# Optimization experiments

Measured on AMD Instinct MI355X. Metric: run time of the kernel, lower is better.

Reference implementation:

```python
import jax, jax.numpy as jnp
import numpy as np

EMB = 2048
N_HEADS = 16
HEAD_DIM = EMB // N_HEADS
ROPE_BASE = 10000.0


def _rope_cos_sin(seq_len, head_dim, dtype):
    inv_freq = 1.0 / (ROPE_BASE ** (jnp.arange(0, head_dim, 2, dtype=jnp.float32) / head_dim))
    t = jnp.arange(seq_len, dtype=jnp.float32)
    freqs = jnp.einsum('s,d->sd', t, inv_freq)          # [S, head_dim/2]
    emb = jnp.concatenate([freqs, freqs], axis=-1)       # [S, head_dim]
    return jnp.cos(emb).astype(dtype), jnp.sin(emb).astype(dtype)


def _rotate_half(x):
    x1, x2 = jnp.split(x, 2, axis=-1)
    return jnp.concatenate([-x2, x1], axis=-1)


def _apply_rope(x, cos, sin):
    # x: [B, H, S, D]; cos/sin: [S, D]
    return x * cos[None, None, :, :] + _rotate_half(x) * sin[None, None, :, :]


def setup_inputs() -> dict:
    key = jax.random.key(0)
    k1, k2, k3 = jax.random.split(key, 3)
    B, S = 4, 2048
    x = jax.random.normal(k1, (B, S, EMB), dtype=jnp.float32)
    # Additive causal mask: 0 on/below diagonal, -1e9 above.
    causal = jnp.triu(jnp.full((S, S), -1e9, dtype=jnp.float32), k=1)
    att_mask = causal[None, None, :, :]
    Wqkv = jax.random.normal(k2, (3 * EMB, EMB), dtype=jnp.float32) * (EMB ** -0.5)
    Wout = jax.random.normal(k3, (EMB, EMB), dtype=jnp.float32) * (EMB ** -0.5)
    return {"x": x, "att_mask": att_mask, "Wqkv": Wqkv, "Wout": Wout}


def reference(x, att_mask, Wqkv, Wout):
    B, S, E = x.shape
    qkv = jnp.einsum('bse,fe->bsf', x, Wqkv)             # [B, S, 3E]
    q, k, v = jnp.split(qkv, 3, axis=-1)
    def to_heads(t):
        return t.reshape(B, S, N_HEADS, HEAD_DIM).transpose(0, 2, 1, 3)  # [B,H,S,D]
    q, k, v = to_heads(q), to_heads(k), to_heads(v)
    cos, sin = _rope_cos_sin(S, HEAD_DIM, x.dtype)
    q = _apply_rope(q, cos, sin)
    k = _apply_rope(k, cos, sin)
    scaling = HEAD_DIM ** -0.5
    dots = jnp.einsum('bhqd,bhkd->bhqk', q, k) * scaling
    dots = dots + att_mask
    attn = jax.nn.softmax(dots, axis=-1)
    out = jnp.einsum('bhqk,bhkd->bhqd', attn, v)         # [B,H,S,D]
    out = out.transpose(0, 2, 1, 3).reshape(B, S, E)
    return jnp.einsum('bse,fe->bsf', out, Wout)
```

## Files before the change

kernel.cpp:

```cpp
#include <hip/hip_runtime.h>
#include <stdint.h>

typedef __attribute__((ext_vector_type(8))) short short8_t;
typedef __attribute__((ext_vector_type(4))) float f32x4;

__device__ __forceinline__ short f2bf(float f) {
  union { float f; uint32_t u; } v; v.f = f;
  uint32_t r = v.u + 0x7FFFu + ((v.u >> 16) & 1u);
  return (short)(r >> 16);
}
__device__ __forceinline__ float bf2f(short s) {
  union { uint32_t u; float f; } v; v.u = ((uint32_t)(uint16_t)s) << 16; return v.f;
}
__device__ __forceinline__ void gld16(const void* g, void* l) {
  __builtin_amdgcn_global_load_lds((const __attribute__((address_space(1))) void*)g,
                                   (__attribute__((address_space(3))) void*)l, 16, 0, 0);
}

__global__ __launch_bounds__(256) void conv_kernel(const float* __restrict__ in,
                                                   short* __restrict__ out, int n4) {
  int i = blockIdx.x * 256 + threadIdx.x;
  const int stride = gridDim.x * 256;
  for (; i < n4; i += stride) {
    float4 v = reinterpret_cast<const float4*>(in)[i];
    short4 o;
    o.x = f2bf(v.x); o.y = f2bf(v.y); o.z = f2bf(v.z); o.w = f2bf(v.w);
    reinterpret_cast<short4*>(out)[i] = o;
  }
}

__device__ __forceinline__ void storeC(float* C, size_t i, float v) { C[i] = v; }
__device__ __forceinline__ void storeC(short* C, size_t i, float v) { C[i] = f2bf(v); }

template <typename OT>
__global__ __launch_bounds__(256) void gemm_bt(const short* __restrict__ A,
                                               const short* __restrict__ B,
                                               OT* __restrict__ C, int M, int N, int K,
                                               int nbx) {
  __shared__ __align__(16) short Al[128 * 32];
  __shared__ __align__(16) short Bl[128 * 32];
  const int tid = threadIdx.x, lane = tid & 63, w = tid >> 6;
  const int wr = w >> 1, wc = w & 1;
  const int c = lane & 15, g4 = lane >> 4;
  const int lin = (blockIdx.x & 7) * ((int)gridDim.x >> 3) + ((int)blockIdx.x >> 3);
  const int bx = lin % nbx, by = lin / nbx;
  const size_t m0 = (size_t)by * 128, n0 = (size_t)bx * 128;
  const size_t Kb = (size_t)K * 2;
  const char* Ab = (const char*)A + m0 * Kb;
  const char* Bb = (const char*)B + n0 * Kb;
  f32x4 acc[4][4] = {};
  const int nk = K >> 5;
  for (int ks = 0; ks < nk; ++ks) {
    const int kb = ks * 64;
#pragma unroll
    for (int i = 0; i < 2; ++i) {
      const int L = ((w * 2 + i) << 10) + lane * 16;
      const int row = L >> 6, inner = L & 63;
      gld16(Ab + (size_t)row * Kb + kb + inner, (char*)Al + ((w * 2 + i) << 10));
      gld16(Bb + (size_t)row * Kb + kb + inner, (char*)Bl + ((w * 2 + i) << 10));
    }
    __syncthreads();
    short8_t af[4], bfr[4];
#pragma unroll
    for (int m = 0; m < 4; ++m)
      af[m] = *(const short8_t*)&Al[(wr * 64 + m * 16 + c) * 32 + g4 * 8];
#pragma unroll
    for (int n = 0; n < 4; ++n)
      bfr[n] = *(const short8_t*)&Bl[(wc * 64 + n * 16 + c) * 32 + g4 * 8];
    __builtin_amdgcn_s_setprio(1);
#pragma unroll
    for (int m = 0; m < 4; ++m)
#pragma unroll
      for (int n = 0; n < 4; ++n)
        acc[m][n] = __builtin_amdgcn_mfma_f32_16x16x32_bf16(af[m], bfr[n], acc[m][n], 0, 0, 0);
    __builtin_amdgcn_s_setprio(0);
    __syncthreads();
  }
#pragma unroll
  for (int m = 0; m < 4; ++m)
#pragma unroll
    for (int n = 0; n < 4; ++n) {
      const size_t col = n0 + wc * 64 + n * 16 + c;
      const size_t rb = m0 + wr * 64 + m * 16 + g4 * 4;
#pragma unroll
      for (int r = 0; r < 4; ++r) storeC(C, (rb + r) * (size_t)N + col, acc[m][n][r]);
    }
}

__global__ __launch_bounds__(256) void rope_kernel(short* __restrict__ qkv) {
  const int g = blockIdx.x * 256 + threadIdx.x;
  const int jg = g & 7;
  const int h = (g >> 3) & 15;
  const int bs = g >> 7;
  const int s = bs & 2047;
  const size_t base = (size_t)bs * 6144 + 2048 + h * 128 + jg * 8;
  short8_t lo = *(short8_t*)&qkv[base];
  short8_t hi = *(short8_t*)&qkv[base + 64];
  short8_t olo, ohi;
#pragma unroll
  for (int t = 0; t < 8; ++t) {
    const int j = jg * 8 + t;
    const float inv = exp2f((float)j * -0.20762050593046f);
    float sn, cn;
    sincosf((float)s * inv, &sn, &cn);
    const float a = bf2f(lo[t]), b = bf2f(hi[t]);
    olo[t] = f2bf(a * cn - b * sn);
    ohi[t] = f2bf(b * cn + a * sn);
  }
  *(short8_t*)&qkv[base] = olo;
  *(short8_t*)&qkv[base + 64] = ohi;
}

__global__ __launch_bounds__(256) void vt_kernel(const short* __restrict__ qkv,
                                                 short* __restrict__ vt) {
  __shared__ __align__(16) short Vl[64][128];
  const int g = blockIdx.x;
  const int st = g & 31, bh = g >> 5;
  const int h = bh & 15, b = bh >> 4;
  const int t = threadIdx.x;
  const int s0 = st * 64;
#pragma unroll
  for (int p = 0; p < 4; ++p) {
    const int idx = p * 256 + t;
    const int row = idx >> 4, c16 = idx & 15;
    short8_t v = *(const short8_t*)&qkv[(size_t)(b * 2048 + s0 + row) * 6144 + 4096 + h * 128 + c16 * 8];
    *(short8_t*)&Vl[row][c16 * 8] = v;
  }
  __syncthreads();
  const size_t obase = ((size_t)(b * 16 + h) * 128) * 2048;
#pragma unroll
  for (int i = 0; i < 8; ++i) {
    const int idx = t * 8 + i;
    const int d = idx >> 4, sq = idx & 15;
    short4 o;
    o.x = Vl[sq * 4 + 0][d];
    o.y = Vl[sq * 4 + 1][d];
    o.z = Vl[sq * 4 + 2][d];
    o.w = Vl[sq * 4 + 3][d];
    *(short4*)&vt[obase + (size_t)d * 2048 + s0 + sq * 4] = o;
  }
}

__global__ __launch_bounds__(256) void attn_kernel(const short* __restrict__ qkv,
                                                   const short* __restrict__ vt,
                                                   short* __restrict__ o) {
  __shared__ __align__(16) short Kl[2][64 * 128];
  __shared__ __align__(16) short Vl[2][128 * 64];
  __shared__ __align__(16) short Pl[4][16 * 72];
  const int tid = threadIdx.x, lane = tid & 63, w = tid >> 6;
  const int c = lane & 15, g4 = lane >> 4;
  const int blk = blockIdx.x;
  const int xcd = blk & 7;
  const int l = blk >> 3;
  const int bh = xcd * 8 + (l >> 5);
  const int h = bh & 15, b = bh >> 4;
  const int q0 = (31 - (l & 31)) * 64;
  const int srow = q0 + w * 16 + c;

  short8_t qf[4];
  {
    const size_t qr = ((size_t)b * 2048 + srow) * 6144 + h * 128;
    float fl[4][8];
#pragma unroll
    for (int dc = 0; dc < 4; ++dc) {
      short8_t rawv = *(const short8_t*)&qkv[qr + dc * 32 + g4 * 8];
#pragma unroll
      for (int t = 0; t < 8; ++t) fl[dc][t] = bf2f(rawv[t]);
    }
#pragma unroll
    for (int pd = 0; pd < 2; ++pd)
#pragma unroll
      for (int t = 0; t < 8; ++t) {
        const int j = pd * 32 + g4 * 8 + t;
        const float inv = exp2f((float)j * -0.20762050593046f);
        float sn, cn;
        sincosf((float)srow * inv, &sn, &cn);
        const float a = fl[pd][t], bb = fl[pd + 2][t];
        fl[pd][t] = a * cn - bb * sn;
        fl[pd + 2][t] = bb * cn + a * sn;
      }
#pragma unroll
    for (int dc = 0; dc < 4; ++dc) {
      short8_t q8;
#pragma unroll
      for (int t = 0; t < 8; ++t) q8[t] = f2bf(fl[dc][t]);
      qf[dc] = q8;
    }
  }

  f32x4 acc_o[8] = {};
  float rs[4] = {0.f, 0.f, 0.f, 0.f};
  const float scale2 = 0.12751875222364685f;
  const char* Kbase = (const char*)qkv + ((size_t)b * 2048 * 6144 + 2048 + h * 128) * 2;
  const char* Vbase = (const char*)vt + ((size_t)(b * 16 + h) * 128 * 2048) * 2;

  const char* kq[4];
  const char* vq[4];
#pragma unroll
  for (int i = 0; i < 4; ++i) {
    const int L = ((w * 4 + i) << 10) + lane * 16;
    {
      const int row = L >> 8, inner = L & 255;
      kq[i] = Kbase + (size_t)row * 12288 + (inner ^ ((row & 7) << 4));
    }
    {
      const int row = L >> 7, inner = L & 127;
      vq[i] = Vbase + (size_t)row * 4096 + (inner ^ ((row & 7) << 4));
    }
  }
  auto stage = [&](int buf, int kv0) {
#pragma unroll
    for (int i = 0; i < 4; ++i) {
      gld16(kq[i] + (size_t)kv0 * 12288, (char*)Kl + (buf << 14) + ((w * 4 + i) << 10));
      gld16(vq[i] + (size_t)kv0 * 2, (char*)Vl + (buf << 14) + ((w * 4 + i) << 10));
    }
  };

  stage(0, 0);
  __syncthreads();
  int cur = 0;
  for (int kv0 = 0; kv0 <= q0; kv0 += 64) {
    if (kv0 + 64 <= q0) stage(cur ^ 1, kv0 + 64);
    const char* Kb = (const char*)Kl + (cur << 14);
    const char* Vb = (const char*)Vl + (cur << 14);
    const bool diag = (kv0 == q0);
    float p[4][4];
#pragma unroll
    for (int kt = 0; kt < 4; ++kt) {
      f32x4 s4 = {};
      const int krow = kt * 16 + c;
      __builtin_amdgcn_s_setprio(1);
#pragma unroll
      for (int dc = 0; dc < 4; ++dc) {
        const int inner = (dc * 64 + g4 * 16) ^ ((krow & 7) << 4);
        short8_t kf = *(const short8_t*)(Kb + krow * 256 + inner);
        s4 = __builtin_amdgcn_mfma_f32_16x16x32_bf16(qf[dc], kf, s4, 0, 0, 0);
      }
      __builtin_amdgcn_s_setprio(0);
#pragma unroll
      for (int r = 0; r < 4; ++r) {
        float v = s4[r] * scale2 - 8.0f;
        if (diag) {
          const int kc = kv0 + kt * 16 + c;
          const int qr2 = q0 + w * 16 + g4 * 4 + r;
          if (kc > qr2) v = -1e30f;
        }
        const float pe = exp2f(v);
        p[kt][r] = pe;
        rs[r] += pe;
      }
    }
#pragma unroll
    for (int kt = 0; kt < 4; ++kt)
#pragma unroll
      for (int r = 0; r < 4; r += 2) {
        uint32_t pk;
        asm("v_cvt_pk_bf16_f32 %0, %1, %2" : "=v"(pk) : "v"(p[kt][r]), "v"(p[kt][r + 1]));
        Pl[w][(g4 * 4 + r) * 72 + kt * 16 + c] = (short)(pk & 0xffffu);
        Pl[w][(g4 * 4 + r + 1) * 72 + kt * 16 + c] = (short)(pk >> 16);
      }
#pragma unroll
    for (int kk = 0; kk < 2; ++kk) {
      short8_t pf = *(const short8_t*)&Pl[w][c * 72 + kk * 32 + g4 * 8];
      __builtin_amdgcn_s_setprio(1);
#pragma unroll
      for (int dt = 0; dt < 8; ++dt) {
        const int vrow = dt * 16 + c;
        const int inner = (kk * 64 + g4 * 16) ^ ((vrow & 7) << 4);
        short8_t vf = *(const short8_t*)(Vb + vrow * 128 + inner);
        acc_o[dt] = __builtin_amdgcn_mfma_f32_16x16x32_bf16(pf, vf, acc_o[dt], 0, 0, 0);
      }
      __builtin_amdgcn_s_setprio(0);
    }
    __syncthreads();
    cur ^= 1;
  }
#pragma unroll
  for (int off = 1; off < 16; off <<= 1)
#pragma unroll
    for (int r = 0; r < 4; ++r) rs[r] += __shfl_xor(rs[r], off);
  const size_t ob = ((size_t)b * 2048 + q0 + w * 16 + g4 * 4) * 2048 + h * 128;
#pragma unroll
  for (int dt = 0; dt < 8; ++dt)
#pragma unroll
    for (int r = 0; r < 4; ++r)
      o[ob + (size_t)r * 2048 + dt * 16 + c] = f2bf(acc_o[dt][r] / rs[r]);
}

extern "C" void kernel_launch(void* const* d_in, const int* in_sizes, int n_in,
                              void* d_out, int out_size, void* d_ws, size_t ws_size,
                              hipStream_t stream) {
  const float* x = (const float*)d_in[0];
  const float* Wqkv = (const float*)d_in[2];
  const float* Wout = (const float*)d_in[3];
  float* out = (float*)d_out;
  char* ws = (char*)d_ws;
  short* xb   = (short*)ws;
  short* wqb  = (short*)(ws + 33554432ull);
  short* qkv  = (short*)(ws + 58720256ull);
  short* vt   = (short*)(ws + 159383552ull);
  short* attno = xb;
  short* woutb = wqb;

  conv_kernel<<<2048, 256, 0, stream>>>(x, xb, 16777216 / 4);
  conv_kernel<<<2048, 256, 0, stream>>>(Wqkv, wqb, 12582912 / 4);
  gemm_bt<short><<<48 * 64, 256, 0, stream>>>(xb, wqb, qkv, 8192, 6144, 2048, 48);
  conv_kernel<<<2048, 256, 0, stream>>>(Wout, woutb, 4194304 / 4);
  rope_kernel<<<4096, 256, 0, stream>>>(qkv);
  vt_kernel<<<2048, 256, 0, stream>>>(qkv, vt);
  attn_kernel<<<2048, 256, 0, stream>>>(qkv, vt, attno);
  gemm_bt<float><<<16 * 64, 256, 0, stream>>>(attno, woutb, out, 8192, 2048, 2048, 16);
}
```

Measured before the change: 585.9 us.

## Use 256x256 double-buffered GEMM tiles with fragment-major LDS layout

Replaces the 128x128, 256-thread GEMM with a 256x256-tile, 512-thread kernel using a K-step of 64. It double-buffers LDS so the next tile's global-to-LDS loads are issued before the MFMAs on the current tile. It also stores operands in a fragment-major LDS layout so each lane reads contiguous 16-byte chunks. The larger tiles raise arithmetic intensity and cut global traffic, but use 128KB of LDS per block, which limits occupancy to one block per CU and reduces the grid to 768 and 256 blocks.

```diff
diff --git a/kernel.cpp b/kernel.cpp
--- a/kernel.cpp
+++ b/kernel.cpp
@@ -33,55 +33,81 @@
 __device__ __forceinline__ void storeC(short* C, size_t i, float v) { C[i] = f2bf(v); }
 
 template <typename OT>
-__global__ __launch_bounds__(256) void gemm_bt(const short* __restrict__ A,
-                                               const short* __restrict__ B,
-                                               OT* __restrict__ C, int M, int N, int K,
-                                               int nbx) {
-  __shared__ __align__(16) short Al[128 * 32];
-  __shared__ __align__(16) short Bl[128 * 32];
+__global__ __launch_bounds__(512, 2) void gemm_bt256(const short* __restrict__ A,
+                                                     const short* __restrict__ B,
+                                                     OT* __restrict__ C, int M, int N, int K,
+                                                     int nbx) {
+  __shared__ __align__(16) short Al[2][256 * 64];
+  __shared__ __align__(16) short Bl[2][256 * 64];
   const int tid = threadIdx.x, lane = tid & 63, w = tid >> 6;
-  const int wr = w >> 1, wc = w & 1;
+  const int wr = w >> 2, wc = w & 3;
   const int c = lane & 15, g4 = lane >> 4;
   const int lin = (blockIdx.x & 7) * ((int)gridDim.x >> 3) + ((int)blockIdx.x >> 3);
   const int bx = lin % nbx, by = lin / nbx;
-  const size_t m0 = (size_t)by * 128, n0 = (size_t)bx * 128;
+  const size_t m0 = (size_t)by * 256, n0 = (size_t)bx * 256;
   const size_t Kb = (size_t)K * 2;
   const char* Ab = (const char*)A + m0 * Kb;
   const char* Bb = (const char*)B + n0 * Kb;
-  f32x4 acc[4][4] = {};
-  const int nk = K >> 5;
-  for (int ks = 0; ks < nk; ++ks) {
-    const int kb = ks * 64;
-#pragma unroll
-    for (int i = 0; i < 2; ++i) {
-      const int L = ((w * 2 + i) << 10) + lane * 16;
-      const int row = L >> 6, inner = L & 63;
-      gld16(Ab + (size_t)row * Kb + kb + inner, (char*)Al + ((w * 2 + i) << 10));
-      gld16(Bb + (size_t)row * Kb + kb + inner, (char*)Bl + ((w * 2 + i) << 10));
-    }
-    __syncthreads();
-    short8_t af[4], bfr[4];
-#pragma unroll
-    for (int m = 0; m < 4; ++m)
-      af[m] = *(const short8_t*)&Al[(wr * 64 + m * 16 + c) * 32 + g4 * 8];
+
+  const char* aq[4];
+  const char* bq[4];
+#pragma unroll
+  for (int i = 0; i < 4; ++i) {
+    const int f = i * 8 + w;
+    const size_t roff = (size_t)((f >> 1) * 16 + c) * Kb + (f & 1) * 64 + g4 * 16;
+    aq[i] = Ab + roff;
+    bq[i] = Bb + roff;
+  }
+
+  f32x4 acc[8][4] = {};
+  const int NT = K >> 6;
+
+#pragma unroll
+  for (int i = 0; i < 4; ++i) {
+    gld16(aq[i], (char*)Al + ((i * 8 + w) << 10));
+    gld16(bq[i], (char*)Bl + ((i * 8 + w) << 10));
+  }
+  __syncthreads();
+
+  for (int kt = 0; kt < NT; ++kt) {
+    const int cur = kt & 1, nb = cur ^ 1;
+    const int kbn = (kt + 1 < NT ? kt + 1 : kt) << 7;
+#pragma unroll
+    for (int i = 0; i < 4; ++i) {
+      gld16(aq[i] + kbn, (char*)Al + (nb << 15) + ((i * 8 + w) << 10));
+      gld16(bq[i] + kbn, (char*)Bl + (nb << 15) + ((i * 8 + w) << 10));
+    }
+    const char* Ac = (const char*)Al + (cur << 15) + lane * 16;
+    const char* Bc = (const char*)Bl + (cur << 15) + lane * 16;
+    short8_t bfr[4][2];
 #pragma unroll
     for (int n = 0; n < 4; ++n)
-      bfr[n] = *(const short8_t*)&Bl[(wc * 64 + n * 16 + c) * 32 + g4 * 8];
+#pragma unroll
+      for (int ks = 0; ks < 2; ++ks)
+        bfr[n][ks] = *(const short8_t*)(Bc + ((((wc * 4 + n) * 2) + ks) << 10));
     __builtin_amdgcn_s_setprio(1);
 #pragma unroll
-    for (int m = 0; m < 4; ++m)
+    for (int m = 0; m < 8; ++m) {
+      const char* ab = Ac + (((wr * 8 + m) * 2) << 10);
+      const short8_t af0 = *(const short8_t*)ab;
+      const short8_t af1 = *(const short8_t*)(ab + 1024);
 #pragma unroll
       for (int n = 0; n < 4; ++n)
-        acc[m][n] = __builtin_amdgcn_mfma_f32_16x16x32_bf16(af[m], bfr[n], acc[m][n], 0, 0, 0);
+        acc[m][n] = __builtin_amdgcn_mfma_f32_16x16x32_bf16(af0, bfr[n][0], acc[m][n], 0, 0, 0);
+#pragma unroll
+      for (int n = 0; n < 4; ++n)
+        acc[m][n] = __builtin_amdgcn_mfma_f32_16x16x32_bf16(af1, bfr[n][1], acc[m][n], 0, 0, 0);
+    }
     __builtin_amdgcn_s_setprio(0);
     __syncthreads();
   }
-#pragma unroll
-  for (int m = 0; m < 4; ++m)
+
+#pragma unroll
+  for (int m = 0; m < 8; ++m)
 #pragma unroll
     for (int n = 0; n < 4; ++n) {
       const size_t col = n0 + wc * 64 + n * 16 + c;
-      const size_t rb = m0 + wr * 64 + m * 16 + g4 * 4;
+      const size_t rb = m0 + wr * 128 + m * 16 + g4 * 4;
 #pragma unroll
       for (int r = 0; r < 4; ++r) storeC(C, (rb + r) * (size_t)N + col, acc[m][n][r]);
     }
@@ -304,10 +330,10 @@
 
   conv_kernel<<<2048, 256, 0, stream>>>(x, xb, 16777216 / 4);
   conv_kernel<<<2048, 256, 0, stream>>>(Wqkv, wqb, 12582912 / 4);
-  gemm_bt<short><<<48 * 64, 256, 0, stream>>>(xb, wqb, qkv, 8192, 6144, 2048, 48);
+  gemm_bt256<short><<<768, 512, 0, stream>>>(xb, wqb, qkv, 8192, 6144, 2048, 24);
   conv_kernel<<<2048, 256, 0, stream>>>(Wout, woutb, 4194304 / 4);
   rope_kernel<<<4096, 256, 0, stream>>>(qkv);
   vt_kernel<<<2048, 256, 0, stream>>>(qkv, vt);
   attn_kernel<<<2048, 256, 0, stream>>>(qkv, vt, attno);
-  gemm_bt<float><<<16 * 64, 256, 0, stream>>>(attno, woutb, out, 8192, 2048, 2048, 16);
-}
+  gemm_bt256<float><<<256, 512, 0, stream>>>(attno, woutb, out, 8192, 2048, 2048, 8);
+}
```

After: 635.8 us. 8.5% more time.

## Replace GEMM with 256x256-tile 8-wave kernel with multi-stage LDS pipelining

Applied to the files above, without the earlier changes.

Replaces the simple 128x128 single-buffered GEMM with a 256x256-tile kernel that uses 8 waves and a 128KB LDS ring. Global-to-LDS loads are prefetched several k-steps ahead, with explicit vmcnt waits and barriers, and interleaved with inline-asm ds_reads and MFMA phases. This is meant to hide global memory latency and raise data reuse per block for both the QKV and output projections. In exchange it adds complex hand-scheduled synchronisation, needs very large LDS, and gives fewer blocks in flight.

```diff
diff --git a/kernel.cpp b/kernel.cpp
--- a/kernel.cpp
+++ b/kernel.cpp
@@ -33,55 +33,117 @@
 __device__ __forceinline__ void storeC(short* C, size_t i, float v) { C[i] = f2bf(v); }
 
 template <typename OT>
-__global__ __launch_bounds__(256) void gemm_bt(const short* __restrict__ A,
-                                               const short* __restrict__ B,
-                                               OT* __restrict__ C, int M, int N, int K,
-                                               int nbx) {
-  __shared__ __align__(16) short Al[128 * 32];
-  __shared__ __align__(16) short Bl[128 * 32];
+__global__ __launch_bounds__(512, 2) void gemm8p(const short* __restrict__ A,
+                                                 const short* __restrict__ B,
+                                                 OT* __restrict__ C, int M, int N, int K,
+                                                 int nbx) {
+  __shared__ __align__(16) short lds[65536];
   const int tid = threadIdx.x, lane = tid & 63, w = tid >> 6;
-  const int wr = w >> 1, wc = w & 1;
+  const int wr = w >> 2, wc = w & 3;
   const int c = lane & 15, g4 = lane >> 4;
   const int lin = (blockIdx.x & 7) * ((int)gridDim.x >> 3) + ((int)blockIdx.x >> 3);
   const int bx = lin % nbx, by = lin / nbx;
-  const size_t m0 = (size_t)by * 128, n0 = (size_t)bx * 128;
+  const size_t m0 = (size_t)by * 256, n0 = (size_t)bx * 256;
   const size_t Kb = (size_t)K * 2;
   const char* Ab = (const char*)A + m0 * Kb;
   const char* Bb = (const char*)B + n0 * Kb;
-  f32x4 acc[4][4] = {};
-  const int nk = K >> 5;
-  for (int ks = 0; ks < nk; ++ks) {
-    const int kb = ks * 64;
-#pragma unroll
-    for (int i = 0; i < 2; ++i) {
-      const int L = ((w * 2 + i) << 10) + lane * 16;
-      const int row = L >> 6, inner = L & 63;
-      gld16(Ab + (size_t)row * Kb + kb + inner, (char*)Al + ((w * 2 + i) << 10));
-      gld16(Bb + (size_t)row * Kb + kb + inner, (char*)Bl + ((w * 2 + i) << 10));
-    }
-    __syncthreads();
-    short8_t af[4], bfr[4];
-#pragma unroll
-    for (int m = 0; m < 4; ++m)
-      af[m] = *(const short8_t*)&Al[(wr * 64 + m * 16 + c) * 32 + g4 * 8];
-#pragma unroll
-    for (int n = 0; n < 4; ++n)
-      bfr[n] = *(const short8_t*)&Bl[(wc * 64 + n * 16 + c) * 32 + g4 * 8];
-    __builtin_amdgcn_s_setprio(1);
-#pragma unroll
-    for (int m = 0; m < 4; ++m)
-#pragma unroll
-      for (int n = 0; n < 4; ++n)
-        acc[m][n] = __builtin_amdgcn_mfma_f32_16x16x32_bf16(af[m], bfr[n], acc[m][n], 0, 0, 0);
-    __builtin_amdgcn_s_setprio(0);
-    __syncthreads();
-  }
-#pragma unroll
-  for (int m = 0; m < 4; ++m)
+  const char* aq[2];
+  const char* bq[2];
+#pragma unroll
+  for (int i = 0; i < 2; ++i) {
+    const size_t ro = (size_t)((i * 8 + w) * 16 + c) * Kb + g4 * 16;
+    aq[i] = Ab + ro;
+    bq[i] = Bb + ro;
+  }
+  char* alds = (char*)lds;
+  const int aoff = wr * 8192 + lane * 16;
+  const int boff = 65536 + wc * 4096 + lane * 16;
+  f32x4 acc[8][4] = {};
+  const int NT = K >> 6, NIT = NT >> 1;
+
+#define STAGE(q, srcoff, ldsbase)                                  \
+  gld16((q)[0] + (srcoff), alds + (ldsbase) + (w << 10));          \
+  gld16((q)[1] + (srcoff), alds + (ldsbase) + ((8 + w) << 10))
+
+  STAGE(aq, 0, 0);
+  STAGE(bq, 0, 65536);
+  STAGE(aq, 64, 16384);
+  STAGE(bq, 64, 81920);
+  STAGE(aq, 128, 32768);
+  STAGE(bq, 128, 98304);
+  asm volatile("s_waitcnt vmcnt(0)" ::: "memory");
+  asm volatile("s_barrier" ::: "memory");
+
+  short8_t af[4], bfr[4];
+
+#define RD_A(mi, OFF) \
+  asm volatile("ds_read_b128 %0, %1 offset:%c2" : "=v"(af[mi]) : "v"(aoff), "i"(OFF))
+#define RD_B(ni, OFF) \
+  asm volatile("ds_read_b128 %0, %1 offset:%c2" : "=v"(bfr[ni]) : "v"(boff), "i"(OFF))
+
+#define MFMA16(MQ)                                                                       \
+  __builtin_amdgcn_s_setprio(1);                                                         \
+  _Pragma("unroll") for (int mi = 0; mi < 4; ++mi) {                                     \
+    _Pragma("unroll") for (int n = 0; n < 4; ++n)                                        \
+      acc[(MQ)*4 + mi][n] =                                                              \
+          __builtin_amdgcn_mfma_f32_16x16x32_bf16(af[mi], bfr[n], acc[(MQ)*4 + mi][n],   \
+                                                  0, 0, 0);                              \
+  }                                                                                      \
+  __builtin_amdgcn_s_setprio(0)
+
+#define PH_EVEN(BSEL, KS, q, srcoff, sbase)                        \
+  asm volatile("s_waitcnt vmcnt(8)" ::: "memory");                 \
+  asm volatile("s_barrier" ::: "memory");                          \
+  STAGE(q, srcoff, sbase);                                         \
+  RD_B(0, (BSEL) + (KS)*16384 + 0);                                \
+  RD_B(1, (BSEL) + (KS)*16384 + 1024);                             \
+  RD_B(2, (BSEL) + (KS)*16384 + 2048);                             \
+  RD_B(3, (BSEL) + (KS)*16384 + 3072);                             \
+  RD_A(0, (BSEL) + (KS)*16384 + 0 * 1024);                         \
+  RD_A(1, (BSEL) + (KS)*16384 + 1 * 1024);                         \
+  RD_A(2, (BSEL) + (KS)*16384 + 2 * 1024);                         \
+  RD_A(3, (BSEL) + (KS)*16384 + 3 * 1024);                         \
+  asm volatile("s_waitcnt lgkmcnt(0)" ::: "memory");               \
+  __builtin_amdgcn_sched_barrier(0);                               \
+  MFMA16(0)
+
+#define PH_ODD(BSEL, KS, q, srcoff, sbase)                         \
+  STAGE(q, srcoff, sbase);                                         \
+  RD_A(0, (BSEL) + (KS)*16384 + 4 * 1024);                         \
+  RD_A(1, (BSEL) + (KS)*16384 + 5 * 1024);                         \
+  RD_A(2, (BSEL) + (KS)*16384 + 6 * 1024);                         \
+  RD_A(3, (BSEL) + (KS)*16384 + 7 * 1024);                         \
+  asm volatile("s_waitcnt lgkmcnt(0)" ::: "memory");               \
+  __builtin_amdgcn_sched_barrier(0);                               \
+  MFMA16(1)
+
+  for (int it = 0; it < NIT; ++it) {
+    const int T = it << 1;
+    const int t1 = (T + 1) << 7;
+    const int t2 = (T + 2 < NT ? T + 2 : NT - 1) << 7;
+    const int t3 = (T + 3 < NT ? T + 3 : NT - 1) << 7;
+    PH_EVEN(0, 0, aq, t1 + 64, 49152);
+    PH_ODD (0, 0, bq, t1 + 64, 114688);
+    PH_EVEN(0, 1, aq, t2, 0);
+    PH_ODD (0, 1, bq, t2, 65536);
+    PH_EVEN(32768, 0, aq, t2 + 64, 16384);
+    PH_ODD (32768, 0, bq, t2 + 64, 81920);
+    PH_EVEN(32768, 1, aq, t3, 32768);
+    PH_ODD (32768, 1, bq, t3, 98304);
+  }
+#undef PH_EVEN
+#undef PH_ODD
+#undef MFMA16
+#undef RD_A
+#undef RD_B
+#undef STAGE
+
+#pragma unroll
+  for (int m = 0; m < 8; ++m)
 #pragma unroll
     for (int n = 0; n < 4; ++n) {
       const size_t col = n0 + wc * 64 + n * 16 + c;
-      const size_t rb = m0 + wr * 64 + m * 16 + g4 * 4;
+      const size_t rb = m0 + wr * 128 + m * 16 + g4 * 4;
 #pragma unroll
       for (int r = 0; r < 4; ++r) storeC(C, (rb + r) * (size_t)N + col, acc[m][n][r]);
     }
@@ -304,10 +366,10 @@
 
   conv_kernel<<<2048, 256, 0, stream>>>(x, xb, 16777216 / 4);
   conv_kernel<<<2048, 256, 0, stream>>>(Wqkv, wqb, 12582912 / 4);
-  gemm_bt<short><<<48 * 64, 256, 0, stream>>>(xb, wqb, qkv, 8192, 6144, 2048, 48);
+  gemm8p<short><<<768, 512, 0, stream>>>(xb, wqb, qkv, 8192, 6144, 2048, 24);
   conv_kernel<<<2048, 256, 0, stream>>>(Wout, woutb, 4194304 / 4);
   rope_kernel<<<4096, 256, 0, stream>>>(qkv);
   vt_kernel<<<2048, 256, 0, stream>>>(qkv, vt);
   attn_kernel<<<2048, 256, 0, stream>>>(qkv, vt, attno);
-  gemm_bt<float><<<16 * 64, 256, 0, stream>>>(attno, woutb, out, 8192, 2048, 2048, 16);
-}
+  gemm8p<float><<<256, 512, 0, stream>>>(attno, woutb, out, 8192, 2048, 2048, 8);
+}
```

Measured after the change: 537.0 us. 1.09x faster.

## Use 256x256 double-buffered 32x32 MFMA GEMM and fuse V-transpose into QKV epilogue

Applied to the files above, without the earlier changes.

Replaces the 128x128 single-buffered GEMM with a 256x256 tile, 512-thread kernel using 32x32x16 bf16 MFMA, hand-scheduled LDS reads and double-buffered global->LDS prefetch. The QKV GEMM epilogue now writes the V third directly in transposed layout, removing the separate vt_kernel pass. The aim is higher arithmetic intensity per tile, overlap of loads with MFMA, and less memory traffic. It relies on hand-written asm waitcnt ordering and a grid-to-tile mapping hardcoded for these shapes, and the large tile gives fewer blocks and a heavier register load.

```diff
diff --git a/kernel.cpp b/kernel.cpp
--- a/kernel.cpp
+++ b/kernel.cpp
@@ -3,6 +3,7 @@
 
 typedef __attribute__((ext_vector_type(8))) short short8_t;
 typedef __attribute__((ext_vector_type(4))) float f32x4;
+typedef __attribute__((ext_vector_type(16))) float f32x16;
 
 __device__ __forceinline__ short f2bf(float f) {
   union { float f; uint32_t u; } v; v.f = f;
@@ -32,58 +33,128 @@
 __device__ __forceinline__ void storeC(float* C, size_t i, float v) { C[i] = v; }
 __device__ __forceinline__ void storeC(short* C, size_t i, float v) { C[i] = f2bf(v); }
 
-template <typename OT>
-__global__ __launch_bounds__(256) void gemm_bt(const short* __restrict__ A,
-                                               const short* __restrict__ B,
-                                               OT* __restrict__ C, int M, int N, int K,
-                                               int nbx) {
-  __shared__ __align__(16) short Al[128 * 32];
-  __shared__ __align__(16) short Bl[128 * 32];
+template <typename OT, bool FUSEV>
+__global__ __launch_bounds__(512, 2) void gemm32(const short* __restrict__ A,
+                                                 const short* __restrict__ B,
+                                                 OT* __restrict__ C,
+                                                 short* __restrict__ VT,
+                                                 int M, int N, int K) {
+  __shared__ __align__(16) short lds[65536];
   const int tid = threadIdx.x, lane = tid & 63, w = tid >> 6;
-  const int wr = w >> 1, wc = w & 1;
-  const int c = lane & 15, g4 = lane >> 4;
-  const int lin = (blockIdx.x & 7) * ((int)gridDim.x >> 3) + ((int)blockIdx.x >> 3);
-  const int bx = lin % nbx, by = lin / nbx;
-  const size_t m0 = (size_t)by * 128, n0 = (size_t)bx * 128;
+  const int wr = w >> 2, wc = w & 3;
+  const int l31 = lane & 31, hl = lane >> 5;
+  const int xcd = (int)blockIdx.x & 7;
+  const int t = (int)blockIdx.x >> 3;
+  const int bx = (t & 7) + 8 * (t >> 5);
+  const int by = xcd * 4 + ((t >> 3) & 3);
+  const size_t m0 = (size_t)by * 256, n0 = (size_t)bx * 256;
   const size_t Kb = (size_t)K * 2;
-  const char* Ab = (const char*)A + m0 * Kb;
-  const char* Bb = (const char*)B + n0 * Kb;
-  f32x4 acc[4][4] = {};
-  const int nk = K >> 5;
-  for (int ks = 0; ks < nk; ++ks) {
-    const int kb = ks * 64;
-#pragma unroll
-    for (int i = 0; i < 2; ++i) {
-      const int L = ((w * 2 + i) << 10) + lane * 16;
-      const int row = L >> 6, inner = L & 63;
-      gld16(Ab + (size_t)row * Kb + kb + inner, (char*)Al + ((w * 2 + i) << 10));
-      gld16(Bb + (size_t)row * Kb + kb + inner, (char*)Bl + ((w * 2 + i) << 10));
-    }
-    __syncthreads();
-    short8_t af[4], bfr[4];
-#pragma unroll
-    for (int m = 0; m < 4; ++m)
-      af[m] = *(const short8_t*)&Al[(wr * 64 + m * 16 + c) * 32 + g4 * 8];
-#pragma unroll
-    for (int n = 0; n < 4; ++n)
-      bfr[n] = *(const short8_t*)&Bl[(wc * 64 + n * 16 + c) * 32 + g4 * 8];
-    __builtin_amdgcn_s_setprio(1);
-#pragma unroll
-    for (int m = 0; m < 4; ++m)
-#pragma unroll
-      for (int n = 0; n < 4; ++n)
-        acc[m][n] = __builtin_amdgcn_mfma_f32_16x16x32_bf16(af[m], bfr[n], acc[m][n], 0, 0, 0);
-    __builtin_amdgcn_s_setprio(0);
-    __syncthreads();
-  }
+  const char* aqp = (const char*)A + (m0 + w * 32 + l31) * Kb + hl * 16;
+  const char* bqp = (const char*)B + (n0 + w * 32 + l31) * Kb + hl * 16;
+  char* alds = (char*)lds;
+  const int aoff = wr * 16384 + lane * 16;
+  const int boff = 65536 + wc * 8192 + lane * 16;
+  f32x16 acc[4][2] = {};
+  const int NT = K >> 6, NIT = NT >> 1;
+
+  short8_t a0, a1, a2, a3, b0, b1, c0, c1, c2, c3, d0, d1;
+
+#define RD_A(reg, IMM) \
+  asm volatile("ds_read_b128 %0, %1 offset:%c2" : "=v"(reg) : "v"(aoff), "i"(IMM))
+#define RD_B(reg, IMM) \
+  asm volatile("ds_read_b128 %0, %1 offset:%c2" : "=v"(reg) : "v"(boff), "i"(IMM))
+
+#define MFMA8(A0, A1, A2, A3, B0, B1)                                          \
+  acc[0][0] = __builtin_amdgcn_mfma_f32_32x32x16_bf16(A0, B0, acc[0][0], 0, 0, 0); \
+  acc[0][1] = __builtin_amdgcn_mfma_f32_32x32x16_bf16(A0, B1, acc[0][1], 0, 0, 0); \
+  acc[1][0] = __builtin_amdgcn_mfma_f32_32x32x16_bf16(A1, B0, acc[1][0], 0, 0, 0); \
+  acc[1][1] = __builtin_amdgcn_mfma_f32_32x32x16_bf16(A1, B1, acc[1][1], 0, 0, 0); \
+  acc[2][0] = __builtin_amdgcn_mfma_f32_32x32x16_bf16(A2, B0, acc[2][0], 0, 0, 0); \
+  acc[2][1] = __builtin_amdgcn_mfma_f32_32x32x16_bf16(A2, B1, acc[2][1], 0, 0, 0); \
+  acc[3][0] = __builtin_amdgcn_mfma_f32_32x32x16_bf16(A3, B0, acc[3][0], 0, 0, 0); \
+  acc[3][1] = __builtin_amdgcn_mfma_f32_32x32x16_bf16(A3, B1, acc[3][1], 0, 0, 0)
+
+  gld16(aqp + 0, alds + ((w * 4 + 0) << 10));
+  gld16(aqp + 32, alds + ((w * 4 + 1) << 10));
+  gld16(bqp + 0, alds + 65536 + ((w * 4 + 0) << 10));
+  gld16(bqp + 32, alds + 65536 + ((w * 4 + 1) << 10));
+  gld16(aqp + 64, alds + ((w * 4 + 2) << 10));
+  gld16(aqp + 96, alds + ((w * 4 + 3) << 10));
+  gld16(bqp + 64, alds + 65536 + ((w * 4 + 2) << 10));
+  gld16(bqp + 96, alds + 65536 + ((w * 4 + 3) << 10));
+
+#define PH(KSL, CB, PT)                                                          \
+  asm volatile("s_waitcnt vmcnt(4)" ::: "memory");                               \
+  asm volatile("s_barrier" ::: "memory");                                        \
+  RD_A(a0, (CB) + 0 * 4096 + (KSL) * 1024);                                      \
+  RD_A(a1, (CB) + 1 * 4096 + (KSL) * 1024);                                      \
+  RD_A(a2, (CB) + 2 * 4096 + (KSL) * 1024);                                      \
+  RD_A(a3, (CB) + 3 * 4096 + (KSL) * 1024);                                      \
+  RD_B(b0, (CB) + 0 * 4096 + (KSL) * 1024);                                      \
+  RD_B(b1, (CB) + 1 * 4096 + (KSL) * 1024);                                      \
+  RD_A(c0, (CB) + 0 * 4096 + ((KSL) + 1) * 1024);                                \
+  RD_A(c1, (CB) + 1 * 4096 + ((KSL) + 1) * 1024);                                \
+  RD_A(c2, (CB) + 2 * 4096 + ((KSL) + 1) * 1024);                                \
+  RD_A(c3, (CB) + 3 * 4096 + ((KSL) + 1) * 1024);                                \
+  RD_B(d0, (CB) + 0 * 4096 + ((KSL) + 1) * 1024);                                \
+  RD_B(d1, (CB) + 1 * 4096 + ((KSL) + 1) * 1024);                                \
+  gld16(aqp + (PT) + (KSL) * 32, alds + ((CB) ^ 32768) + ((w * 4 + (KSL)) << 10));       \
+  gld16(aqp + (PT) + ((KSL) + 1) * 32, alds + ((CB) ^ 32768) + ((w * 4 + (KSL) + 1) << 10)); \
+  gld16(bqp + (PT) + (KSL) * 32, alds + 65536 + ((CB) ^ 32768) + ((w * 4 + (KSL)) << 10));   \
+  gld16(bqp + (PT) + ((KSL) + 1) * 32, alds + 65536 + ((CB) ^ 32768) + ((w * 4 + (KSL) + 1) << 10)); \
+  asm volatile("s_waitcnt lgkmcnt(6)" ::: "memory");                             \
+  __builtin_amdgcn_sched_barrier(0);                                             \
+  __builtin_amdgcn_s_setprio(1);                                                 \
+  MFMA8(a0, a1, a2, a3, b0, b1);                                                 \
+  __builtin_amdgcn_s_setprio(0);                                                 \
+  asm volatile("s_waitcnt lgkmcnt(0)" ::: "memory");                             \
+  __builtin_amdgcn_sched_barrier(0);                                             \
+  __builtin_amdgcn_s_setprio(1);                                                 \
+  MFMA8(c0, c1, c2, c3, d0, d1);                                                 \
+  __builtin_amdgcn_s_setprio(0)
+
+  for (int it = 0; it < NIT; ++it) {
+    const int T = it << 1;
+    const int p1 = (T + 1) << 7;
+    const int p2 = (T + 2 < NT ? T + 2 : NT - 1) << 7;
+    PH(0, 0, p1);
+    PH(2, 0, p1);
+    PH(0, 32768, p2);
+    PH(2, 32768, p2);
+  }
+#undef PH
+#undef MFMA8
+#undef RD_A
+#undef RD_B
+
 #pragma unroll
   for (int m = 0; m < 4; ++m)
 #pragma unroll
-    for (int n = 0; n < 4; ++n) {
-      const size_t col = n0 + wc * 64 + n * 16 + c;
-      const size_t rb = m0 + wr * 64 + m * 16 + g4 * 4;
-#pragma unroll
-      for (int r = 0; r < 4; ++r) storeC(C, (rb + r) * (size_t)N + col, acc[m][n][r]);
+    for (int n = 0; n < 2; ++n) {
+      const size_t col = n0 + wc * 64 + n * 32 + l31;
+      const int rbase = (int)m0 + wr * 128 + m * 32 + hl * 4;
+      bool tovt = false;
+      if constexpr (FUSEV) tovt = (col >= 4096);
+      if (tovt) {
+        const size_t cc = col - 4096;
+        const size_t bb = (size_t)(rbase >> 11);
+#pragma unroll
+        for (int j = 0; j < 4; ++j) {
+          const int s0 = (rbase & 2047) + j * 8;
+          short4 o;
+          o.x = f2bf(acc[m][n][j * 4 + 0]);
+          o.y = f2bf(acc[m][n][j * 4 + 1]);
+          o.z = f2bf(acc[m][n][j * 4 + 2]);
+          o.w = f2bf(acc[m][n][j * 4 + 3]);
+          *(short4*)&VT[(bb * 2048 + cc) * 2048 + s0] = o;
+        }
+      } else {
+#pragma unroll
+        for (int j = 0; j < 4; ++j)
+#pragma unroll
+          for (int r = 0; r < 4; ++r)
+            storeC(C, (size_t)(rbase + j * 8 + r) * (size_t)N + col, acc[m][n][j * 4 + r]);
+      }
     }
 }
 
@@ -109,36 +180,6 @@
   }
   *(short8_t*)&qkv[base] = olo;
   *(short8_t*)&qkv[base + 64] = ohi;
-}
-
-__global__ __launch_bounds__(256) void vt_kernel(const short* __restrict__ qkv,
-                                                 short* __restrict__ vt) {
-  __shared__ __align__(16) short Vl[64][128];
-  const int g = blockIdx.x;
-  const int st = g & 31, bh = g >> 5;
-  const int h = bh & 15, b = bh >> 4;
-  const int t = threadIdx.x;
-  const int s0 = st * 64;
-#pragma unroll
-  for (int p = 0; p < 4; ++p) {
-    const int idx = p * 256 + t;
-    const int row = idx >> 4, c16 = idx & 15;
-    short8_t v = *(const short8_t*)&qkv[(size_t)(b * 2048 + s0 + row) * 6144 + 4096 + h * 128 + c16 * 8];
-    *(short8_t*)&Vl[row][c16 * 8] = v;
-  }
-  __syncthreads();
-  const size_t obase = ((size_t)(b * 16 + h) * 128) * 2048;
-#pragma unroll
-  for (int i = 0; i < 8; ++i) {
-    const int idx = t * 8 + i;
-    const int d = idx >> 4, sq = idx & 15;
-    short4 o;
-    o.x = Vl[sq * 4 + 0][d];
-    o.y = Vl[sq * 4 + 1][d];
-    o.z = Vl[sq * 4 + 2][d];
-    o.w = Vl[sq * 4 + 3][d];
-    *(short4*)&vt[obase + (size_t)d * 2048 + s0 + sq * 4] = o;
-  }
 }
 
 __global__ __launch_bounds__(256) void attn_kernel(const short* __restrict__ qkv,
@@ -304,10 +345,9 @@
 
   conv_kernel<<<2048, 256, 0, stream>>>(x, xb, 16777216 / 4);
   conv_kernel<<<2048, 256, 0, stream>>>(Wqkv, wqb, 12582912 / 4);
-  gemm_bt<short><<<48 * 64, 256, 0, stream>>>(xb, wqb, qkv, 8192, 6144, 2048, 48);
+  gemm32<short, true><<<768, 512, 0, stream>>>(xb, wqb, qkv, vt, 8192, 6144, 2048);
   conv_kernel<<<2048, 256, 0, stream>>>(Wout, woutb, 4194304 / 4);
   rope_kernel<<<4096, 256, 0, stream>>>(qkv);
-  vt_kernel<<<2048, 256, 0, stream>>>(qkv, vt);
   attn_kernel<<<2048, 256, 0, stream>>>(qkv, vt, attno);
-  gemm_bt<float><<<16 * 64, 256, 0, stream>>>(attno, woutb, out, 8192, 2048, 2048, 16);
-}
+  gemm32<float, false><<<256, 512, 0, stream>>>(attno, woutb, out, nullptr, 8192, 2048, 2048);
+}
```

Result: faster. 529.9 us (-9.6%).
